# Optimization experiments

Measured on AMD Instinct MI355X. Metric: run time of the kernel, lower is better.

The kernel has to match this reference:

```python
import jax, jax.numpy as jnp
import numpy as np

B, N, FIN, FOUT, H = 8, 2048, 128, 128, 2


def setup_inputs() -> dict:
    key = jax.random.key(0)
    k_h, k_adj, k_w, k_a = jax.random.split(key, 4)
    h = jax.random.normal(k_h, (B, N, FIN), dtype=jnp.float32)
    adj = jax.random.randint(k_adj, (B, N, N), 0, 2).astype(jnp.int32)
    # self-loops so no softmax row is all -inf
    idx = jnp.arange(N)
    adj = adj.at[:, idx, idx].set(1)
    W = jax.random.normal(k_w, (H, FIN, FOUT), dtype=jnp.float32) * 0.1
    a = jax.random.normal(k_a, (H, 2 * FOUT), dtype=jnp.float32) * 0.1
    return {"h": h, "adj": adj, "W": W, "a": a}


def reference(h, adj, W, a):
    # h: [B,N,FIN], adj: [B,N,N] int, W: [H,FIN,FOUT], a: [H,2*FOUT]
    Fout = W.shape[-1]
    Wh = jnp.einsum('bnf,hfo->bhno', h, W)              # [B,H,N,FOUT]
    # decompose a^T [Wh_i || Wh_j] = a1.Wh_i + a2.Wh_j (exact same math,
    # avoids the [B,N,N,2F] concat the torch code materializes)
    a1, a2 = a[:, :Fout], a[:, Fout:]
    s_i = jnp.einsum('bhno,ho->bhn', Wh, a1)            # score from node i
    s_j = jnp.einsum('bhno,ho->bhn', Wh, a2)            # score from node j
    e = jax.nn.leaky_relu(s_i[:, :, :, None] + s_j[:, :, None, :], 0.2)  # [B,H,N,N]
    e = jnp.where(adj[:, None, :, :] == 0, -jnp.inf, e)
    att = jax.nn.softmax(e, axis=-1)                    # [B,H,N,N]
    out = jnp.einsum('bhnm,bhmo->bhno', att, Wh)        # [B,H,N,FOUT]
    b, hh, n, f = out.shape
    # concat heads along feature dim (head order matches torch cat)
    return out.transpose(0, 2, 1, 3).reshape(b, n, hh * f)
```

## Files before the change

### kernel.cpp

```cpp
#include <hip/hip_runtime.h>
#include <math.h>

constexpr int Bv   = 8;
constexpr int Nv   = 2048;
constexpr int FIN  = 128;
constexpr int FOUT = 128;
constexpr int NH   = 2;
constexpr float LOG2E = 1.44269504088896340736f;

typedef __attribute__((ext_vector_type(8)))  short short8;
typedef __attribute__((ext_vector_type(4)))  float f32x4;
typedef __attribute__((ext_vector_type(16))) float f32x16;
typedef __attribute__((ext_vector_type(4)))  int   i32x4;
typedef unsigned long long u64;

static __device__ __forceinline__ unsigned short f2bf(float f) {
    unsigned u = __builtin_bit_cast(unsigned, f);
    u += 0x7fffu + ((u >> 16) & 1u);
    return (unsigned short)(u >> 16);
}
static __device__ __forceinline__ float bf2f(unsigned short s) {
    unsigned u = ((unsigned)s) << 16;
    return __builtin_bit_cast(float, u);
}
static __device__ __forceinline__ float fast_exp2(float x) {
#if __has_builtin(__builtin_amdgcn_exp2f)
    return __builtin_amdgcn_exp2f(x);
#else
    return exp2f(x);
#endif
}
static __device__ __forceinline__ unsigned cvt_pk_bf16(float lo, float hi) {
    unsigned r;
    asm("v_cvt_pk_bf16_f32 %0, %1, %2" : "=v"(r) : "v"(lo), "v"(hi));
    return r;
}

__global__ __launch_bounds__(256) void wa_kernel(const float* __restrict__ W,
                                                 const float* __restrict__ a,
                                                 float* __restrict__ wa,
                                                 unsigned short* __restrict__ wthi,
                                                 unsigned short* __restrict__ wtlo) {
    __shared__ unsigned short shi[FIN * 132];
    __shared__ unsigned short slo[FIN * 132];
    int hh = blockIdx.x;
    int t = threadIdx.x;

    const float* Ws = W + (size_t)hh * FIN * FOUT;
    for (int idx = t; idx < FIN * FOUT; idx += 256) {
        int f = idx >> 7, o = idx & 127;
        float wv = Ws[idx];
        unsigned short uh = f2bf(wv);
        shi[o * 132 + f] = uh;
        slo[o * 132 + f] = f2bf(wv - bf2f(uh));
    }

    int f = t >> 1, half = t & 1;
    const float* Wr = Ws + (size_t)f * FOUT + half * 64;
    const float* ar = a + (size_t)hh * 2 * FOUT + half * 64;
    float s1 = 0.f, s2 = 0.f;
    for (int o = 0; o < 64; o += 4) {
        float4 w4 = *(const float4*)&Wr[o];
        s1 += w4.x * ar[o] + w4.y * ar[o + 1] + w4.z * ar[o + 2] + w4.w * ar[o + 3];
        s2 += w4.x * ar[FOUT + o] + w4.y * ar[FOUT + o + 1] + w4.z * ar[FOUT + o + 2] + w4.w * ar[FOUT + o + 3];
    }
    s1 += __shfl_xor(s1, 1, 64);
    s2 += __shfl_xor(s2, 1, 64);
    if (half == 0) {
        wa[(hh * 2 + 0) * FIN + f] = s1 * LOG2E;
        wa[(hh * 2 + 1) * FIN + f] = s2 * LOG2E;
    }

    __syncthreads();
    unsigned short* dhi = wthi + (size_t)hh * FOUT * FIN;
    unsigned short* dlo = wtlo + (size_t)hh * FOUT * FIN;
    for (int idx = t; idx < FIN * FOUT; idx += 256) {
        int o = idx >> 7, ff = idx & 127;
        dhi[idx] = shi[o * 132 + ff];
        dlo[idx] = slo[o * 132 + ff];
    }
}

__global__ __launch_bounds__(256, 4) void prep_kernel(
    const float* __restrict__ h, const int* __restrict__ adj,
    const float* __restrict__ wa,
    const unsigned short* __restrict__ wthi, const unsigned short* __restrict__ wtlo,
    u64* __restrict__ adjp, unsigned short* __restrict__ whf,
    float* __restrict__ si, float* __restrict__ sj) {
    __shared__ u64 plds[64][33];

    int bid = blockIdx.x;
    int t   = threadIdx.x;

    if (bid < 256) {
        int wv = t >> 6, l = t & 63;
        int gb    = bid >> 5;
        int rbase = (bid & 31) * 64 + wv * 16;
        const int* src = adj + ((size_t)gb * Nv + rbase) * Nv + l;
        for (int r = 0; r < 16; ++r) {
            const int* rp = src + (size_t)r * Nv;
#pragma unroll
            for (int jt8 = 0; jt8 < 32; jt8 += 8) {
                int av[8];
#pragma unroll
                for (int k = 0; k < 8; ++k) av[k] = rp[(jt8 + k) * 64];
                u64 mm[8];
#pragma unroll
                for (int k = 0; k < 8; ++k) mm[k] = __ballot(av[k] != 0);
                if (l == 0) {
#pragma unroll
                    for (int k = 0; k < 8; ++k) plds[wv * 16 + r][jt8 + k] = mm[k];
                }
            }
        }
        __syncthreads();
        int n0B = (bid & 31) * 64;
#pragma unroll
        for (int i = 0; i < 8; ++i) {
            int idx = i * 256 + t;
            int jt = idx >> 6, row = idx & 63;
            adjp[((size_t)gb * 32 + jt) * Nv + n0B + row] = plds[row][jt];
        }
    } else if (bid < 4352) {
        int row  = (bid - 256) * 4 + (t >> 6);
        int lane = t & 63;
        float x0 = h[(size_t)row * FIN + lane];
        float x1 = h[(size_t)row * FIN + 64 + lane];
        float s[4];
#pragma unroll
        for (int q = 0; q < 4; ++q) {
            const float* wp = wa + q * FIN;
            s[q] = x0 * wp[lane] + x1 * wp[64 + lane];
        }
#pragma unroll
        for (int m = 32; m >= 1; m >>= 1) {
#pragma unroll
            for (int q = 0; q < 4; ++q) s[q] += __shfl_xor(s[q], m, 64);
        }
        if (lane == 0) {
            int bb = row >> 11, n = row & (Nv - 1);
            si[((size_t)(bb * NH + 0)) * Nv + n] = s[0];
            sj[((size_t)(bb * NH + 0)) * Nv + n] = s[1];
            si[((size_t)(bb * NH + 1)) * Nv + n] = s[2];
            sj[((size_t)(bb * NH + 1)) * Nv + n] = s[3];
        }
    } else {
        int wb2 = bid - 4352;
        int bb  = wb2 & 7;
        int r2  = wb2 >> 3;
        int hh  = r2 & 1;
        int jtb = r2 >> 1;
        int n0  = jtb * 64;

        int w = t >> 6, l = t & 63, lo16 = l & 15, grp = l >> 4;
        int o0 = w * 32;

        const unsigned short* Whi = wthi + (size_t)hh * FOUT * FIN;
        const unsigned short* Wlo = wtlo + (size_t)hh * FOUT * FIN;
        short8 ahi[2][4], alo[2][4];
#pragma unroll
        for (int ot = 0; ot < 2; ++ot)
#pragma unroll
            for (int kt = 0; kt < 4; ++kt) {
                int off = (o0 + ot * 16 + lo16) * FIN + kt * 32 + grp * 8;
                ahi[ot][kt] = *(const short8*)&Whi[off];
                alo[ot][kt] = *(const short8*)&Wlo[off];
            }

        f32x4 acc[2][4];
#pragma unroll
        for (int ot = 0; ot < 2; ++ot)
#pragma unroll
            for (int nt = 0; nt < 4; ++nt) acc[ot][nt] = (f32x4){0.f, 0.f, 0.f, 0.f};

        const float* hb = h + ((size_t)bb * Nv + n0) * FIN;
#pragma unroll
        for (int nt = 0; nt < 4; ++nt) {
#pragma unroll
            for (int kt = 0; kt < 4; ++kt) {
                const float* hp = hb + (size_t)(nt * 16 + lo16) * FIN + kt * 32 + grp * 8;
                float4 x0 = *(const float4*)hp;
                float4 x1 = *(const float4*)(hp + 4);
                float xs[8] = {x0.x, x0.y, x0.z, x0.w, x1.x, x1.y, x1.z, x1.w};
                short8 bhi, blo;
#pragma unroll
                for (int i = 0; i < 8; ++i) {
                    unsigned short uh = f2bf(xs[i]);
                    bhi[i] = (short)uh;
                    blo[i] = (short)f2bf(xs[i] - bf2f(uh));
                }
#pragma unroll
                for (int ot = 0; ot < 2; ++ot) {
                    acc[ot][nt] = __builtin_amdgcn_mfma_f32_16x16x32_bf16(ahi[ot][kt], bhi, acc[ot][nt], 0, 0, 0);
                    acc[ot][nt] = __builtin_amdgcn_mfma_f32_16x16x32_bf16(ahi[ot][kt], blo, acc[ot][nt], 0, 0, 0);
                    acc[ot][nt] = __builtin_amdgcn_mfma_f32_16x16x32_bf16(alo[ot][kt], bhi, acc[ot][nt], 0, 0, 0);
                }
            }
        }
        unsigned short* db = whf + (size_t)(bb * NH + hh) * 262144;
#pragma unroll
        for (int ot = 0; ot < 2; ++ot)
#pragma unroll
            for (int nt = 0; nt < 4; ++nt)
#pragma unroll
                for (int reg = 0; reg < 4; ++reg) {
                    int oc = ot * 16 + grp * 4 + reg;
                    db[(size_t)(((jtb * 4 + nt) * 4 + w) * 64 + (lo16 >> 3) * 32 + oc) * 8 + (lo16 & 7)] =
                        f2bf(acc[ot][nt][reg]);
                }
    }
}

__global__ __launch_bounds__(256, 3) void gat_attn_kernel(
    const u64* __restrict__ adjp, const unsigned short* __restrict__ whf,
    const float* __restrict__ si, const float* __restrict__ sj,
    float* __restrict__ out) {
    int bid = blockIdx.x;
    int bb  = bid & 7;
    int r2  = bid >> 3;
    int rp  = r2 & 31;
    int hh  = (r2 >> 5) & 1;
    int ch  = r2 >> 6;

    int t = threadIdx.x, w = t >> 6, l = t & 63;
    int jp = w & 1, rw = w >> 1;
    int lo32 = l & 31, kh = l >> 5;
    int r0 = rp * 64 + rw * 32;
    int myrow = r0 + lo32;

    float sir = si[(size_t)(bb * NH + hh) * Nv + myrow];
    const u64*   adjr = adjp + (size_t)bb * 32 * Nv + myrow;
    const float* sjb  = sj + (size_t)(bb * NH + hh) * Nv;
    const unsigned short* wbp = whf + (size_t)(bb * NH + hh) * 262144 + (size_t)l * 8;

    f32x16 acc0, acc1, accL;
#pragma unroll
    for (int i = 0; i < 16; ++i) { acc0[i] = 0.f; acc1[i] = 0.f; accL[i] = 0.f; }

    const int ones_w = 0x3f803f80;
    short8 onesf = __builtin_bit_cast(short8, (i32x4){ones_w, ones_w, ones_w, ones_w});

    int jt0 = jp * 16;
    u64 mask = adjr[(size_t)jt0 * Nv];
    for (int jtl = 0; jtl < 16; ++jtl) {
        int jt = jt0 + jtl;
        int jb = jt * 64;
        const unsigned short* fb = wbp + (size_t)(jt * 16 + ch * 2) * 512;
        short8 bf[4][2];
#pragma unroll
        for (int kt = 0; kt < 4; ++kt) {
            bf[kt][0] = *(const short8*)(fb + (kt * 4 + 0) * 512);
            bf[kt][1] = *(const short8*)(fb + (kt * 4 + 1) * 512);
        }
        u64 mcur = mask;
        if (jtl < 15) mask = adjr[(size_t)(jt + 1) * Nv];

        short8 af[4];
#pragma unroll
        for (int kt = 0; kt < 4; ++kt) {
            unsigned mb = (unsigned)(mcur >> (kt * 16 + kh * 8)) & 0xFFu;
            const float* sp = &sjb[jb + kt * 16 + kh * 8];
            float4 s0 = *(const float4*)sp;
            float4 s1 = *(const float4*)(sp + 4);
            float x0 = sir + s0.x, x1 = sir + s0.y, x2 = sir + s0.z, x3 = sir + s0.w;
            float x4 = sir + s1.x, x5 = sir + s1.y, x6 = sir + s1.z, x7 = sir + s1.w;
            x0 = fmaxf(x0, 0.2f * x0); x1 = fmaxf(x1, 0.2f * x1);
            x2 = fmaxf(x2, 0.2f * x2); x3 = fmaxf(x3, 0.2f * x3);
            x4 = fmaxf(x4, 0.2f * x4); x5 = fmaxf(x5, 0.2f * x5);
            x6 = fmaxf(x6, 0.2f * x6); x7 = fmaxf(x7, 0.2f * x7);
            float p0 = fast_exp2(x0), p1 = fast_exp2(x1), p2 = fast_exp2(x2), p3 = fast_exp2(x3);
            float p4 = fast_exp2(x4), p5 = fast_exp2(x5), p6 = fast_exp2(x6), p7 = fast_exp2(x7);
            p0 = (mb & 1u)   ? p0 : 0.f;  p1 = (mb & 2u)   ? p1 : 0.f;
            p2 = (mb & 4u)   ? p2 : 0.f;  p3 = (mb & 8u)   ? p3 : 0.f;
            p4 = (mb & 16u)  ? p4 : 0.f;  p5 = (mb & 32u)  ? p5 : 0.f;
            p6 = (mb & 64u)  ? p6 : 0.f;  p7 = (mb & 128u) ? p7 : 0.f;
            unsigned w0 = cvt_pk_bf16(p0, p1), w1 = cvt_pk_bf16(p2, p3);
            unsigned w2 = cvt_pk_bf16(p4, p5), w3 = cvt_pk_bf16(p6, p7);
            af[kt] = __builtin_bit_cast(short8, (i32x4){(int)w0, (int)w1, (int)w2, (int)w3});
        }
#pragma unroll
        for (int kt = 0; kt < 4; ++kt) {
            acc0 = __builtin_amdgcn_mfma_f32_32x32x16_bf16(af[kt], bf[kt][0], acc0, 0, 0, 0);
            acc1 = __builtin_amdgcn_mfma_f32_32x32x16_bf16(af[kt], bf[kt][1], acc1, 0, 0, 0);
            accL = __builtin_amdgcn_mfma_f32_32x32x16_bf16(af[kt], onesf,    accL, 0, 0, 0);
        }
    }

    __shared__ float red[2][64][49];
    if (jp == 1) {
#pragma unroll
        for (int i = 0; i < 16; ++i) {
            red[rw][l][i]      = acc0[i];
            red[rw][l][16 + i] = acc1[i];
            red[rw][l][32 + i] = accL[i];
        }
    }
    __syncthreads();
    if (jp == 0) {
#pragma unroll
        for (int i = 0; i < 16; ++i) {
            acc0[i] += red[rw][l][i];
            acc1[i] += red[rw][l][16 + i];
            accL[i] += red[rw][l][32 + i];
        }
#pragma unroll
        for (int reg = 0; reg < 16; ++reg) {
            int rowc = (reg & 3) + 8 * (reg >> 2) + 4 * kh;
            float linv = 1.0f / accL[reg];
            float* op = out + ((size_t)(bb * Nv + r0 + rowc)) * (NH * FOUT) + hh * FOUT + ch * 64;
            op[lo32]      = acc0[reg] * linv;
            op[32 + lo32] = acc1[reg] * linv;
        }
    }
}

extern "C" void kernel_launch(void* const* d_in, const int* in_sizes, int n_in,
                              void* d_out, int out_size, void* d_ws, size_t ws_size,
                              hipStream_t stream) {
    const float* h   = (const float*)d_in[0];
    const int*   adj = (const int*)d_in[1];
    const float* W   = (const float*)d_in[2];
    const float* a   = (const float*)d_in[3];
    float*       out = (float*)d_out;

    char* ws = (char*)d_ws;
    unsigned short* whf  = (unsigned short*)ws;
    u64*            adjp = (u64*)(ws + 8388608);
    float* si = (float*)(ws + 8388608 + 4194304);
    float* sj = si + (size_t)Bv * NH * Nv;
    float* wa = sj + (size_t)Bv * NH * Nv;
    unsigned short* wthi = (unsigned short*)(wa + NH * 2 * FIN);
    unsigned short* wtlo = wthi + (size_t)NH * FOUT * FIN;

    wa_kernel  <<<dim3(2),    dim3(256), 0, stream>>>(W, a, wa, wthi, wtlo);
    prep_kernel<<<dim3(4864), dim3(256), 0, stream>>>(h, adj, wa, wthi, wtlo, adjp, whf, si, sj);
    gat_attn_kernel<<<dim3(1024), dim3(256), 0, stream>>>(adjp, whf, si, sj, out);
}
```

Measured before the change: 106.1 us.

## Vectorize adjacency packing with int4 loads and permute neighbor order consistently

Each lane of the adjacency-packing pass now reads four consecutive int32 entries with one 16-byte load, instead of issuing strided scalar loads. This changes which column each ballot bit maps to, so the neighbor index is effectively permuted. The s_j write-out and the packed Wh layout are remapped to the same permutation, which keeps the softmax and aggregation in the unchanged attention kernel consistent. Packing blocks now cover 32 rows each instead of 64, so the grid has twice as many of them. The aim is faster streaming of the large int32 adjacency tensor, at the cost of coupled index remapping that must stay in sync across three buffers.

```diff
diff --git a/kernel.cpp b/kernel.cpp
--- a/kernel.cpp
+++ b/kernel.cpp
@@ -13,6 +13,7 @@
 typedef __attribute__((ext_vector_type(16))) float f32x16;
 typedef __attribute__((ext_vector_type(4)))  int   i32x4;
 typedef unsigned long long u64;
+
 
 static __device__ __forceinline__ unsigned short f2bf(float f) {
     unsigned u = __builtin_bit_cast(unsigned, f);
@@ -87,42 +88,45 @@
     const unsigned short* __restrict__ wthi, const unsigned short* __restrict__ wtlo,
     u64* __restrict__ adjp, unsigned short* __restrict__ whf,
     float* __restrict__ si, float* __restrict__ sj) {
-    __shared__ u64 plds[64][33];
+    __shared__ u64 plds[32][33];
 
     int bid = blockIdx.x;
     int t   = threadIdx.x;
 
-    if (bid < 256) {
+    if (bid < 512) {
         int wv = t >> 6, l = t & 63;
-        int gb    = bid >> 5;
-        int rbase = (bid & 31) * 64 + wv * 16;
-        const int* src = adj + ((size_t)gb * Nv + rbase) * Nv + l;
-        for (int r = 0; r < 16; ++r) {
+        int gb    = bid >> 6;
+        int rbase = (bid & 63) * 32 + wv * 8;
+        const int* src = adj + ((size_t)gb * Nv + rbase) * Nv + l * 4;
+        for (int r = 0; r < 8; ++r) {
             const int* rp = src + (size_t)r * Nv;
-#pragma unroll
-            for (int jt8 = 0; jt8 < 32; jt8 += 8) {
-                int av[8];
-#pragma unroll
-                for (int k = 0; k < 8; ++k) av[k] = rp[(jt8 + k) * 64];
-                u64 mm[8];
-#pragma unroll
-                for (int k = 0; k < 8; ++k) mm[k] = __ballot(av[k] != 0);
+            int4 av[8];
+#pragma unroll
+            for (int c = 0; c < 8; ++c) av[c] = *(const int4*)&rp[c * 256];
+#pragma unroll
+            for (int c = 0; c < 8; ++c) {
+                u64 b0 = __ballot(av[c].x != 0);
+                u64 b1 = __ballot(av[c].y != 0);
+                u64 b2 = __ballot(av[c].z != 0);
+                u64 b3 = __ballot(av[c].w != 0);
                 if (l == 0) {
-#pragma unroll
-                    for (int k = 0; k < 8; ++k) plds[wv * 16 + r][jt8 + k] = mm[k];
+                    plds[wv * 8 + r][c * 4 + 0] = b0;
+                    plds[wv * 8 + r][c * 4 + 1] = b1;
+                    plds[wv * 8 + r][c * 4 + 2] = b2;
+                    plds[wv * 8 + r][c * 4 + 3] = b3;
                 }
             }
         }
         __syncthreads();
-        int n0B = (bid & 31) * 64;
-#pragma unroll
-        for (int i = 0; i < 8; ++i) {
+        int n0B = (bid & 63) * 32;
+#pragma unroll
+        for (int i = 0; i < 4; ++i) {
             int idx = i * 256 + t;
-            int jt = idx >> 6, row = idx & 63;
-            adjp[((size_t)gb * 32 + jt) * Nv + n0B + row] = plds[row][jt];
-        }
-    } else if (bid < 4352) {
-        int row  = (bid - 256) * 4 + (t >> 6);
+            int tt = idx >> 5, row = idx & 31;
+            adjp[((size_t)gb * 32 + tt) * Nv + n0B + row] = plds[row][tt];
+        }
+    } else if (bid < 4608) {
+        int row  = (bid - 512) * 4 + (t >> 6);
         int lane = t & 63;
         float x0 = h[(size_t)row * FIN + lane];
         float x1 = h[(size_t)row * FIN + 64 + lane];
@@ -139,13 +143,14 @@
         }
         if (lane == 0) {
             int bb = row >> 11, n = row & (Nv - 1);
-            si[((size_t)(bb * NH + 0)) * Nv + n] = s[0];
-            sj[((size_t)(bb * NH + 0)) * Nv + n] = s[1];
-            si[((size_t)(bb * NH + 1)) * Nv + n] = s[2];
-            sj[((size_t)(bb * NH + 1)) * Nv + n] = s[3];
+            int np = (n & ~255) | ((n & 3) << 6) | ((n >> 2) & 63);
+            si[((size_t)(bb * NH + 0)) * Nv + n]  = s[0];
+            sj[((size_t)(bb * NH + 0)) * Nv + np] = s[1];
+            si[((size_t)(bb * NH + 1)) * Nv + n]  = s[2];
+            sj[((size_t)(bb * NH + 1)) * Nv + np] = s[3];
         }
     } else {
-        int wb2 = bid - 4352;
+        int wb2 = bid - 4608;
         int bb  = wb2 & 7;
         int r2  = wb2 >> 3;
         int hh  = r2 & 1;
@@ -198,6 +203,9 @@
             }
         }
         unsigned short* db = whf + (size_t)(bb * NH + hh) * 262144;
+        int tt   = 4 * (jtb >> 2) + (lo16 & 3);
+        int kt2  = jtb & 3;
+        int i2b  = lo16 >> 2;
 #pragma unroll
         for (int ot = 0; ot < 2; ++ot)
 #pragma unroll
@@ -205,7 +213,8 @@
 #pragma unroll
                 for (int reg = 0; reg < 4; ++reg) {
                     int oc = ot * 16 + grp * 4 + reg;
-                    db[(size_t)(((jtb * 4 + nt) * 4 + w) * 64 + (lo16 >> 3) * 32 + oc) * 8 + (lo16 & 7)] =
+                    int i2 = (nt & 1) * 4 + i2b;
+                    db[(size_t)((((tt * 4 + kt2) * 4 + w) * 64 + ((nt >> 1) & 1) * 32 + oc)) * 8 + i2] =
                         f2bf(acc[ot][nt][reg]);
                 }
     }
@@ -333,6 +342,6 @@
     unsigned short* wtlo = wthi + (size_t)NH * FOUT * FIN;
 
     wa_kernel  <<<dim3(2),    dim3(256), 0, stream>>>(W, a, wa, wthi, wtlo);
-    prep_kernel<<<dim3(4864), dim3(256), 0, stream>>>(h, adj, wa, wthi, wtlo, adjp, whf, si, sj);
+    prep_kernel<<<dim3(5120), dim3(256), 0, stream>>>(h, adj, wa, wthi, wtlo, adjp, whf, si, sj);
     gat_attn_kernel<<<dim3(1024), dim3(256), 0, stream>>>(adjp, whf, si, sj, out);
 }
```

Result: slower. 114.5 us (+7.9%).
